# Kernel tuning notes

Hardware: AMD Instinct MI355X
Metric: run time of the kernel (lower is better)

The kernel has to match this reference:

```python
import jax, jax.numpy as jnp
import numpy as np

B, S, E, NH = 2, 2048, 1024, 4
HD = E // NH  # 256


def setup_inputs() -> dict:
    key = jax.random.key(0)
    ks = jax.random.split(key, 8)
    return {
        "q": jax.random.normal(ks[0], (B, S, E), jnp.float32),
        "k": jax.random.normal(ks[1], (B, S, E), jnp.float32),
        "v": jax.random.normal(ks[2], (B, S, E), jnp.float32),
        # gate Dense params (kernel zero-init in the module; use small random for a nontrivial baseline)
        "igate_kernel": jax.random.normal(ks[3], (3 * E, NH), jnp.float32) * 0.02,
        "igate_bias": jax.random.normal(ks[4], (NH,), jnp.float32) * 0.1,
        "fgate_kernel": jax.random.normal(ks[5], (3 * E, NH), jnp.float32) * 0.02,
        "fgate_bias": jnp.linspace(3.0, 6.0, NH, dtype=jnp.float32),  # bias_linspace_init
        "rms_scale": jax.random.normal(ks[6], (HD,), jnp.float32) * 0.02,
    }


def _mlstm_head(q, k, v, ig, fg, eps=1e-06):
    # q,k,v: (S, DH); ig, fg: (S, 1)
    s, dh = q.shape
    log_f = jax.nn.log_sigmoid(fg)                       # (S,1)
    cs = jnp.concatenate([jnp.zeros((1, 1), log_f.dtype),
                          jnp.cumsum(log_f, axis=0)], axis=0)  # (S+1,1)
    neg = jnp.asarray(-0.7 * jnp.finfo(cs.dtype).max, cs.dtype)
    log_d = jnp.where(jnp.tri(s, dtype=bool),
                      (cs - cs.T)[1:, 1:] + ig.T, neg)   # (S,S)
    m = jnp.max(log_d, axis=-1, keepdims=True)           # row-wise stabilizer
    d = jnp.exp(log_d - m)
    c = (q @ (k.T / jnp.sqrt(dh))) * d                   # (S,S)
    n = jnp.maximum(jnp.sum(c, axis=-1, keepdims=True), jnp.exp(-m))
    return (c / (n + eps)) @ v                           # (S,DH)


def reference(q, k, v, igate_kernel, igate_bias, fgate_kernel, fgate_bias, rms_scale):
    b, s, e = q.shape
    nh = igate_kernel.shape[1]
    hd = e // nh
    gate_in = jnp.concatenate((q, k, v), axis=-1)                 # (B,S,3E)
    ig = (gate_in @ igate_kernel + igate_bias).swapaxes(-1, -2)[..., None]  # (B,NH,S,1)
    fg = (gate_in @ fgate_kernel + fgate_bias).swapaxes(-1, -2)[..., None]  # (B,NH,S,1)
    qh = q.reshape(b, s, nh, hd).swapaxes(1, 2)                   # (B,NH,S,HD)
    kh = k.reshape(b, s, nh, hd).swapaxes(1, 2)
    vh = v.reshape(b, s, nh, hd).swapaxes(1, 2)
    h = jax.vmap(jax.vmap(_mlstm_head))(qh, kh, vh, ig, fg)      # (B,NH,S,HD)
    # RMSNorm over head_dim with (1+scale)
    var = jnp.mean(jnp.square(h.astype(jnp.float32)), axis=-1, keepdims=True)
    h = (h * jax.lax.rsqrt(var + 1e-06)).astype(h.dtype) * (1.0 + rms_scale)
    return h.swapaxes(1, 2).reshape(b, s, e)
```

## Files before the change

### kernel.cpp

```cpp
#include <hip/hip_runtime.h>
#include <math.h>

static constexpr int B_  = 2;
static constexpr int S_  = 2048;
static constexpr int E_  = 1024;
static constexpr int NH_ = 4;
static constexpr int HD_ = 256;
static constexpr int BH_ = B_ * NH_;

typedef __attribute__((ext_vector_type(8))) _Float16 half8;
typedef __attribute__((ext_vector_type(4))) float    f32x4;
typedef __attribute__((ext_vector_type(4))) _Float16 half4v;

__global__ __launch_bounds__(1024) void prep_kernel(
    const float* __restrict__ q, const float* __restrict__ k, const float* __restrict__ v,
    const float* __restrict__ igk, const float* __restrict__ igb,
    const float* __restrict__ fgk, const float* __restrict__ fgb,
    float* __restrict__ ig_out, float* __restrict__ fg_out,
    _Float16* __restrict__ Qh, _Float16* __restrict__ Kh, _Float16* __restrict__ Vt)
{
    __shared__ __align__(16) char PSM[98304];
    float4* wi = (float4*)PSM;
    float4* wf = wi + 3 * E_;

    const int t = threadIdx.x;
    #pragma unroll
    for (int i = 0; i < 3; ++i) {
        int e = t + 1024 * i;
        wi[e] = ((const float4*)igk)[e];
        wf[e] = ((const float4*)fgk)[e];
    }
    __syncthreads();

    const int wave = t >> 6;
    const int l    = t & 63;
    const int bs   = blockIdx.x * 16 + wave;
    const int b = bs >> 11, s = bs & (S_ - 1);
    const float* qrow = q + (size_t)bs * E_;
    const float* krow = k + (size_t)bs * E_;
    const float* vrow = v + (size_t)bs * E_;

    float accI[4] = {0.f,0.f,0.f,0.f}, accF[4] = {0.f,0.f,0.f,0.f};
    #pragma unroll
    for (int j = 0; j < 48; ++j) {
        const int e = l + 64 * j;
        float g;
        if (j < 16)       g = qrow[e];
        else if (j < 32)  g = krow[e - E_];
        else              g = vrow[e - 2 * E_];
        if (j < 16) {
            int hh = e >> 8, d = e & 255;
            Qh[(((size_t)(b * NH_ + hh)) * S_ + s) * HD_ + d] = (_Float16)(g * 0.0625f);
        } else if (j < 32) {
            int e2 = e - E_; int hh = e2 >> 8, d = e2 & 255;
            Kh[(((size_t)(b * NH_ + hh)) * S_ + s) * HD_ + d] = (_Float16)g;
        }
        float4 wiv = wi[e];
        float4 wfv = wf[e];
        accI[0] = fmaf(g, wiv.x, accI[0]); accI[1] = fmaf(g, wiv.y, accI[1]);
        accI[2] = fmaf(g, wiv.z, accI[2]); accI[3] = fmaf(g, wiv.w, accI[3]);
        accF[0] = fmaf(g, wfv.x, accF[0]); accF[1] = fmaf(g, wfv.y, accF[1]);
        accF[2] = fmaf(g, wfv.z, accF[2]); accF[3] = fmaf(g, wfv.w, accF[3]);
    }
    #pragma unroll
    for (int m = 1; m < 64; m <<= 1) {
        #pragma unroll
        for (int h = 0; h < 4; ++h) {
            accI[h] += __shfl_xor(accI[h], m);
            accF[h] += __shfl_xor(accF[h], m);
        }
    }
    if (l == 0) {
        #pragma unroll
        for (int h = 0; h < 4; ++h) {
            ig_out[((size_t)(b * NH_ + h)) * S_ + s] = accI[h] + igb[h];
            fg_out[((size_t)(b * NH_ + h)) * S_ + s] = accF[h] + fgb[h];
        }
    }

    __syncthreads();
    {
        float (*tile)[65] = (float(*)[65])(PSM + (t >> 8) * 16640);
        const int tid = t & 255;
        const int m  = blockIdx.x * 4 + (t >> 8);
        const int bh = m & 7;
        const int sb = (m >> 3) & 31;
        const int db = m >> 8;
        const int bb = bh >> 2, hh = bh & 3;
        const int j4 = (tid & 15) * 4;
        const int i0 = tid >> 4;
        const float* src = v + ((size_t)(bb * S_ + sb * 64)) * E_ + hh * HD_ + db * 64;
        #pragma unroll
        for (int p = 0; p < 4; ++p) {
            int i = i0 + p * 16;
            float4 val = *(const float4*)(src + (size_t)i * E_ + j4);
            tile[i][j4] = val.x; tile[i][j4+1] = val.y; tile[i][j4+2] = val.z; tile[i][j4+3] = val.w;
        }
        __syncthreads();
        const int s4 = (tid & 15) * 4;
        const int d0 = tid >> 4;
        _Float16* dst = Vt + ((size_t)bh * HD_ + db * 64) * S_ + sb * 64;
        #pragma unroll
        for (int p = 0; p < 4; ++p) {
            int d = d0 + p * 16;
            half4v pk;
            pk.x = (_Float16)tile[s4][d];   pk.y = (_Float16)tile[s4+1][d];
            pk.z = (_Float16)tile[s4+2][d]; pk.w = (_Float16)tile[s4+3][d];
            *(half4v*)(dst + (size_t)d * S_ + s4) = pk;
        }
    }
}

static constexpr int KSS = 264;
static constexpr int VSS = 72;
static constexpr int PBS = 72;
static constexpr int OFF_VS  = 64 * KSS * 2;
static constexpr int OFF_PB  = OFF_VS + 256 * VSS * 2;
static constexpr int OFF_RSE = OFF_PB + 2 * 16 * PBS * 2;
static constexpr int OFF_SSE = OFF_RSE + 512;
static constexpr int OFF_AMM = OFF_SSE + 512;
static constexpr int OFF_G   = OFF_AMM + S_ * 4;
static constexpr int OFF_M   = OFF_G   + S_ * 4;
static constexpr int SMB     = OFF_M   + S_ * 4;

__global__ __launch_bounds__(512, 2) void mlstm_kernel(
    const _Float16* __restrict__ Qh, const _Float16* __restrict__ Kh,
    const _Float16* __restrict__ Vt,
    const float* __restrict__ ig, const float* __restrict__ fg,
    const float* __restrict__ rms_scale, float* __restrict__ out)
{
    __shared__ __align__(16) char SMEM[SMB];
    _Float16* Ks    = (_Float16*)SMEM;
    _Float16* Vs    = (_Float16*)(SMEM + OFF_VS);
    _Float16* Pb    = (_Float16*)(SMEM + OFF_PB);
    float*    rsumE = (float*)(SMEM + OFF_RSE);
    float*    ssE   = (float*)(SMEM + OFF_SSE);
    float*    sAmM  = (float*)(SMEM + OFF_AMM);
    float*    sG    = (float*)(SMEM + OFF_G);
    float*    sM    = (float*)(SMEM + OFF_M);

    const int z  = blockIdx.x;
    const int bh = z & 7;
    const int u  = z >> 3;
    const int b  = bh >> 2, h = bh & 3;
    const int t  = threadIdx.x;
    const int w  = t >> 6;
    const int l  = t & 63;
    const int col  = l & 15;
    const int quad = l >> 4;
    const int qo   = quad * 8;
    const int rw   = w >> 2;
    const int cq   = w & 3;

    {
        float* sc = (float*)SMEM;
        const float* fgp = fg + (size_t)bh * S_;
        const float* igp = ig + (size_t)bh * S_;
        float ls[4];
        float run = 0.f;
        #pragma unroll
        for (int i = 0; i < 4; ++i) {
            float x = fgp[t * 4 + i];
            float lg = (x >= 0.f) ? -log1pf(expf(-x)) : (x - log1pf(expf(x)));
            run += lg;
            ls[i] = run;
        }
        sc[t] = run;
        __syncthreads();
        for (int off = 1; off < 512; off <<= 1) {
            float vv = (t >= off) ? sc[t - off] : 0.f;
            __syncthreads();
            sc[t] += vv;
            __syncthreads();
        }
        float excl = sc[t] - run;
        float A[4], g[4], gm[4];
        #pragma unroll
        for (int i = 0; i < 4; ++i) A[i] = excl + ls[i];
        float rmax = -__builtin_inff();
        #pragma unroll
        for (int i = 0; i < 4; ++i) {
            g[i] = igp[t * 4 + i] - A[i];
            rmax = fmaxf(rmax, g[i]);
            gm[i] = rmax;
        }
        __syncthreads();
        sc[t] = rmax;
        __syncthreads();
        for (int off = 1; off < 512; off <<= 1) {
            float vv = (t >= off) ? sc[t - off] : -__builtin_inff();
            __syncthreads();
            sc[t] = fmaxf(sc[t], vv);
            __syncthreads();
        }
        float exm = (t == 0) ? -__builtin_inff() : sc[t - 1];
        #pragma unroll
        for (int i = 0; i < 4; ++i) {
            float cm = fmaxf(exm, gm[i]);
            float Mi = A[i] + cm;
            sAmM[t * 4 + i] = A[i] - Mi;
            sG[t * 4 + i]   = g[i];
            sM[t * 4 + i]   = Mi;
        }
        __syncthreads();
    }

    const _Float16* Qp  = Qh + (size_t)bh * S_ * HD_;
    const _Float16* Kp  = Kh + (size_t)bh * S_ * HD_;
    const _Float16* Vtp = Vt + (size_t)bh * HD_ * S_;
    _Float16* Pbr = Pb + rw * 16 * PBS;

    half8 kpre[4], vpre[4];
    auto issueK = [&](int c0n) {
        #pragma unroll
        for (int i = 0; i < 4; ++i) {
            int p = t + 512 * i;
            int row = p >> 5, ck = p & 31;
            kpre[i] = *(const half8*)(Kp + (size_t)(c0n + row) * HD_ + ck * 8);
        }
    };
    auto issueV = [&](int c0n) {
        #pragma unroll
        for (int i = 0; i < 4; ++i) {
            int p = t + 512 * i;
            int n = p >> 3, ch = p & 7;
            vpre[i] = *(const half8*)(Vtp + (size_t)n * S_ + c0n + ch * 8);
        }
    };

    issueK(0);
    issueV(0);

    for (int pass = 0; pass < 2; ++pass) {
        const int rb = pass ? (63 - u) : u;
        const int rowbase = rb * 32 + rw * 16;

        half8 qf[8];
        #pragma unroll
        for (int kk = 0; kk < 8; ++kk)
            qf[kk] = *(const half8*)(Qp + (size_t)(rowbase + col) * HD_ + kk * 32 + qo);
        float amM[4];
        #pragma unroll
        for (int rr = 0; rr < 4; ++rr) amM[rr] = sAmM[rowbase + quad * 4 + rr];

        f32x4 acc[4];
        #pragma unroll
        for (int nn = 0; nn < 4; ++nn) acc[nn] = (f32x4){0.f, 0.f, 0.f, 0.f};
        float rs[4] = {0.f, 0.f, 0.f, 0.f};

        const int Tt = (rb >> 1) + 1;
        for (int jt = 0; jt < Tt; ++jt) {
            const int c0 = jt << 6;
            __syncthreads();
            #pragma unroll
            for (int i = 0; i < 4; ++i) {
                int p = t + 512 * i;
                int row = p >> 5, ck = p & 31;
                *(half8*)(Ks + row * KSS + ck * 8) = kpre[i];
            }
            #pragma unroll
            for (int i = 0; i < 4; ++i) {
                int p = t + 512 * i;
                int n = p >> 3, ch = p & 7;
                *(half8*)(Vs + n * VSS + ch * 8) = vpre[i];
            }
            __syncthreads();
            if (!(pass == 1 && jt + 1 == Tt)) {
                const int cn = (jt + 1 < Tt) ? (c0 + 64) : 0;
                issueK(cn);
                issueV(cn);
            }
            const float gv = sG[c0 + cq * 16 + col];
            f32x4 sc0 = (f32x4){0.f,0.f,0.f,0.f};
            #pragma unroll
            for (int kk = 0; kk < 8; ++kk) {
                half8 kf = *(const half8*)(Ks + (cq * 16 + col) * KSS + kk * 32 + qo);
                sc0 = __builtin_amdgcn_mfma_f32_16x16x32_f16(qf[kk], kf, sc0, 0, 0, 0);
            }
            #pragma unroll
            for (int rr = 0; rr < 4; ++rr) {
                const int ig_ = rowbase + quad * 4 + rr;
                float e0 = __expf(amM[rr] + gv);
                float p0 = (c0 + cq * 16 + col <= ig_) ? sc0[rr] * e0 : 0.f;
                rs[rr] += p0;
                Pbr[(quad * 4 + rr) * PBS + cq * 16 + col] = (_Float16)p0;
            }
            __syncthreads();
            half8 af0 = *(const half8*)(Pbr + col * PBS + qo);
            half8 af1 = *(const half8*)(Pbr + col * PBS + 32 + qo);
            #pragma unroll
            for (int nn = 0; nn < 4; ++nn) {
                const int n = cq * 64 + nn * 16 + col;
                half8 vf0 = *(const half8*)(Vs + n * VSS + qo);
                half8 vf1 = *(const half8*)(Vs + n * VSS + 32 + qo);
                acc[nn] = __builtin_amdgcn_mfma_f32_16x16x32_f16(af0, vf0, acc[nn], 0, 0, 0);
                acc[nn] = __builtin_amdgcn_mfma_f32_16x16x32_f16(af1, vf1, acc[nn], 0, 0, 0);
            }
        }

        #pragma unroll
        for (int m = 1; m < 16; m <<= 1) {
            #pragma unroll
            for (int rr = 0; rr < 4; ++rr) rs[rr] += __shfl_xor(rs[rr], m);
        }
        if (col == 0) {
            #pragma unroll
            for (int rr = 0; rr < 4; ++rr)
                rsumE[rw * 64 + cq * 16 + quad * 4 + rr] = rs[rr];
        }
        __syncthreads();
        float inv[4], ss[4];
        #pragma unroll
        for (int rr = 0; rr < 4; ++rr) {
            const int r = quad * 4 + rr;
            float tot = rsumE[rw * 64 + r] + rsumE[rw * 64 + 16 + r]
                      + rsumE[rw * 64 + 32 + r] + rsumE[rw * 64 + 48 + r];
            float Mv = sM[rowbase + r];
            float n = fmaxf(tot, __expf(-Mv)) + 1e-6f;
            inv[rr] = 1.0f / n;
            ss[rr] = 0.f;
        }
        #pragma unroll
        for (int nn = 0; nn < 4; ++nn) {
            #pragma unroll
            for (int rr = 0; rr < 4; ++rr) {
                float hv = acc[nn][rr] * inv[rr];
                acc[nn][rr] = hv;
                ss[rr] = fmaf(hv, hv, ss[rr]);
            }
        }
        #pragma unroll
        for (int m = 1; m < 16; m <<= 1) {
            #pragma unroll
            for (int rr = 0; rr < 4; ++rr) ss[rr] += __shfl_xor(ss[rr], m);
        }
        if (col == 0) {
            #pragma unroll
            for (int rr = 0; rr < 4; ++rr)
                ssE[rw * 64 + cq * 16 + quad * 4 + rr] = ss[rr];
        }
        __syncthreads();
        #pragma unroll
        for (int rr = 0; rr < 4; ++rr) {
            const int r = quad * 4 + rr;
            float sst = ssE[rw * 64 + r] + ssE[rw * 64 + 16 + r]
                      + ssE[rw * 64 + 32 + r] + ssE[rw * 64 + 48 + r];
            float rstd = rsqrtf(sst * (1.0f / HD_) + 1e-6f);
            float* orow = out + ((size_t)(b * S_ + rowbase + r)) * E_ + h * HD_;
            #pragma unroll
            for (int nn = 0; nn < 4; ++nn) {
                const int c = cq * 64 + nn * 16 + col;
                orow[c] = acc[nn][rr] * rstd * (1.0f + rms_scale[c]);
            }
        }
        __syncthreads();
    }
}

extern "C" void kernel_launch(void* const* d_in, const int* in_sizes, int n_in,
                              void* d_out, int out_size, void* d_ws, size_t ws_size,
                              hipStream_t stream) {
    (void)in_sizes; (void)n_in; (void)out_size; (void)ws_size;
    const float* q   = (const float*)d_in[0];
    const float* k   = (const float*)d_in[1];
    const float* v   = (const float*)d_in[2];
    const float* igk = (const float*)d_in[3];
    const float* igb = (const float*)d_in[4];
    const float* fgk = (const float*)d_in[5];
    const float* fgb = (const float*)d_in[6];
    const float* rsc = (const float*)d_in[7];
    float* out = (float*)d_out;

    float* ws  = (float*)d_ws;
    float* ig  = ws;
    float* fg  = ws + (size_t)BH_ * S_;
    _Float16* Qh = (_Float16*)(ws + (size_t)2 * BH_ * S_);
    _Float16* Kh = Qh + (size_t)BH_ * S_ * HD_;
    _Float16* Vt = Kh + (size_t)BH_ * S_ * HD_;

    prep_kernel<<<B_ * S_ / 16, 1024, 0, stream>>>(q, k, v, igk, igb, fgk, fgb,
                                                   ig, fg, Qh, Kh, Vt);
    mlstm_kernel<<<BH_ * 32, 512, 0, stream>>>(Qh, Kh, Vt, ig, fg, rsc, out);
}
```

Before: 168.5 us.

## Split prep kernel into gate-projection blocks and V-transpose blocks with register-blocked rows

The prep kernel is restructured from 256 blocks of 1024 threads, each staging 96KB of gate weights in shared memory, into 2048 blocks of 256 threads. The first 1024 blocks each compute gate projections for 4 rows using float4 vector loads, read the weights straight from global/cache with reuse across the 4 rows in registers, and reduce across waves through a small shared buffer. The remaining 1024 blocks do the V transpose on their own. This is meant to cut the shared-memory weight staging and raise occupancy and load vectorisation, at the cost of re-reading the weights from cache in every block.

```diff
diff --git a/kernel.cpp b/kernel.cpp
--- a/kernel.cpp
+++ b/kernel.cpp
@@ -12,77 +12,110 @@
 typedef __attribute__((ext_vector_type(4))) float    f32x4;
 typedef __attribute__((ext_vector_type(4))) _Float16 half4v;
 
-__global__ __launch_bounds__(1024) void prep_kernel(
+__global__ __launch_bounds__(256) void prep_kernel(
     const float* __restrict__ q, const float* __restrict__ k, const float* __restrict__ v,
     const float* __restrict__ igk, const float* __restrict__ igb,
     const float* __restrict__ fgk, const float* __restrict__ fgb,
     float* __restrict__ ig_out, float* __restrict__ fg_out,
     _Float16* __restrict__ Qh, _Float16* __restrict__ Kh, _Float16* __restrict__ Vt)
 {
-    __shared__ __align__(16) char PSM[98304];
-    float4* wi = (float4*)PSM;
-    float4* wf = wi + 3 * E_;
-
-    const int t = threadIdx.x;
-    #pragma unroll
-    for (int i = 0; i < 3; ++i) {
-        int e = t + 1024 * i;
-        wi[e] = ((const float4*)igk)[e];
-        wf[e] = ((const float4*)fgk)[e];
-    }
-    __syncthreads();
-
-    const int wave = t >> 6;
-    const int l    = t & 63;
-    const int bs   = blockIdx.x * 16 + wave;
-    const int b = bs >> 11, s = bs & (S_ - 1);
-    const float* qrow = q + (size_t)bs * E_;
-    const float* krow = k + (size_t)bs * E_;
-    const float* vrow = v + (size_t)bs * E_;
-
-    float accI[4] = {0.f,0.f,0.f,0.f}, accF[4] = {0.f,0.f,0.f,0.f};
-    #pragma unroll
-    for (int j = 0; j < 48; ++j) {
-        const int e = l + 64 * j;
-        float g;
-        if (j < 16)       g = qrow[e];
-        else if (j < 32)  g = krow[e - E_];
-        else              g = vrow[e - 2 * E_];
-        if (j < 16) {
-            int hh = e >> 8, d = e & 255;
-            Qh[(((size_t)(b * NH_ + hh)) * S_ + s) * HD_ + d] = (_Float16)(g * 0.0625f);
-        } else if (j < 32) {
-            int e2 = e - E_; int hh = e2 >> 8, d = e2 & 255;
-            Kh[(((size_t)(b * NH_ + hh)) * S_ + s) * HD_ + d] = (_Float16)g;
-        }
-        float4 wiv = wi[e];
-        float4 wfv = wf[e];
-        accI[0] = fmaf(g, wiv.x, accI[0]); accI[1] = fmaf(g, wiv.y, accI[1]);
-        accI[2] = fmaf(g, wiv.z, accI[2]); accI[3] = fmaf(g, wiv.w, accI[3]);
-        accF[0] = fmaf(g, wfv.x, accF[0]); accF[1] = fmaf(g, wfv.y, accF[1]);
-        accF[2] = fmaf(g, wfv.z, accF[2]); accF[3] = fmaf(g, wfv.w, accF[3]);
-    }
-    #pragma unroll
-    for (int m = 1; m < 64; m <<= 1) {
-        #pragma unroll
-        for (int h = 0; h < 4; ++h) {
-            accI[h] += __shfl_xor(accI[h], m);
-            accF[h] += __shfl_xor(accF[h], m);
-        }
-    }
-    if (l == 0) {
-        #pragma unroll
-        for (int h = 0; h < 4; ++h) {
-            ig_out[((size_t)(b * NH_ + h)) * S_ + s] = accI[h] + igb[h];
-            fg_out[((size_t)(b * NH_ + h)) * S_ + s] = accF[h] + fgb[h];
-        }
-    }
-
-    __syncthreads();
-    {
-        float (*tile)[65] = (float(*)[65])(PSM + (t >> 8) * 16640);
-        const int tid = t & 255;
-        const int m  = blockIdx.x * 4 + (t >> 8);
+    __shared__ __align__(16) char PSM[16640];
+    const int tid = threadIdx.x;
+
+    if (blockIdx.x < 1024) {
+        const int bs0 = blockIdx.x * 4;
+        const float4* w_i = (const float4*)igk;
+        const float4* w_f = (const float4*)fgk;
+
+        float accI[4][4], accF[4][4];
+        #pragma unroll
+        for (int r = 0; r < 4; ++r)
+            #pragma unroll
+            for (int h = 0; h < 4; ++h) { accI[r][h] = 0.f; accF[r][h] = 0.f; }
+
+        #pragma unroll
+        for (int it = 0; it < 3; ++it) {
+            const int e4  = tid + 256 * it;
+            const int e4l = e4 & 255;
+            const float* src = (it == 0) ? q : (it == 1) ? k : v;
+
+            float4 g4[4];
+            #pragma unroll
+            for (int r = 0; r < 4; ++r)
+                g4[r] = ((const float4*)(src + (size_t)(bs0 + r) * E_))[e4l];
+
+            if (it == 0) {
+                #pragma unroll
+                for (int r = 0; r < 4; ++r) {
+                    const int bs = bs0 + r, b = bs >> 11, s = bs & (S_ - 1);
+                    half4v hq = { (_Float16)(g4[r].x * 0.0625f), (_Float16)(g4[r].y * 0.0625f),
+                                  (_Float16)(g4[r].z * 0.0625f), (_Float16)(g4[r].w * 0.0625f) };
+                    *(half4v*)(Qh + ((size_t)(b * NH_ + (e4l >> 6)) * S_ + s) * HD_ + (e4l & 63) * 4) = hq;
+                }
+            } else if (it == 1) {
+                #pragma unroll
+                for (int r = 0; r < 4; ++r) {
+                    const int bs = bs0 + r, b = bs >> 11, s = bs & (S_ - 1);
+                    half4v hk = { (_Float16)g4[r].x, (_Float16)g4[r].y,
+                                  (_Float16)g4[r].z, (_Float16)g4[r].w };
+                    *(half4v*)(Kh + ((size_t)(b * NH_ + (e4l >> 6)) * S_ + s) * HD_ + (e4l & 63) * 4) = hk;
+                }
+            }
+
+            float4 wi4[4], wf4[4];
+            #pragma unroll
+            for (int j = 0; j < 4; ++j) {
+                wi4[j] = w_i[e4 * 4 + j];
+                wf4[j] = w_f[e4 * 4 + j];
+            }
+            #pragma unroll
+            for (int r = 0; r < 4; ++r) {
+                const float gx[4] = { g4[r].x, g4[r].y, g4[r].z, g4[r].w };
+                #pragma unroll
+                for (int j = 0; j < 4; ++j) {
+                    accI[r][0] = fmaf(gx[j], wi4[j].x, accI[r][0]);
+                    accI[r][1] = fmaf(gx[j], wi4[j].y, accI[r][1]);
+                    accI[r][2] = fmaf(gx[j], wi4[j].z, accI[r][2]);
+                    accI[r][3] = fmaf(gx[j], wi4[j].w, accI[r][3]);
+                    accF[r][0] = fmaf(gx[j], wf4[j].x, accF[r][0]);
+                    accF[r][1] = fmaf(gx[j], wf4[j].y, accF[r][1]);
+                    accF[r][2] = fmaf(gx[j], wf4[j].z, accF[r][2]);
+                    accF[r][3] = fmaf(gx[j], wf4[j].w, accF[r][3]);
+                }
+            }
+        }
+        #pragma unroll
+        for (int m = 1; m < 64; m <<= 1) {
+            #pragma unroll
+            for (int r = 0; r < 4; ++r)
+                #pragma unroll
+                for (int h = 0; h < 4; ++h) {
+                    accI[r][h] += __shfl_xor(accI[r][h], m);
+                    accF[r][h] += __shfl_xor(accF[r][h], m);
+                }
+        }
+        float (*red)[4][8] = (float(*)[4][8])PSM;
+        const int wave = tid >> 6;
+        if ((tid & 63) == 0) {
+            #pragma unroll
+            for (int r = 0; r < 4; ++r)
+                #pragma unroll
+                for (int h = 0; h < 4; ++h) {
+                    red[wave][r][h]     = accI[r][h];
+                    red[wave][r][4 + h] = accF[r][h];
+                }
+        }
+        __syncthreads();
+        if (tid < 32) {
+            const int r = tid >> 3, c = tid & 7, h = c & 3;
+            float sum = red[0][r][c] + red[1][r][c] + red[2][r][c] + red[3][r][c];
+            const int bs = bs0 + r, b = bs >> 11, s = bs & (S_ - 1);
+            if (c < 4) ig_out[((size_t)(b * NH_ + h)) * S_ + s] = sum + igb[h];
+            else       fg_out[((size_t)(b * NH_ + h)) * S_ + s] = sum + fgb[h];
+        }
+    } else {
+        float (*tile)[65] = (float(*)[65])PSM;
+        const int m  = blockIdx.x - 1024;
         const int bh = m & 7;
         const int sb = (m >> 3) & 31;
         const int db = m >> 8;
@@ -378,7 +411,7 @@
     _Float16* Kh = Qh + (size_t)BH_ * S_ * HD_;
     _Float16* Vt = Kh + (size_t)BH_ * S_ * HD_;
 
-    prep_kernel<<<B_ * S_ / 16, 1024, 0, stream>>>(q, k, v, igk, igb, fgk, fgb,
-                                                   ig, fg, Qh, Kh, Vt);
+    prep_kernel<<<2048, 256, 0, stream>>>(q, k, v, igk, igb, fgk, fgb,
+                                          ig, fg, Qh, Kh, Vt);
     mlstm_kernel<<<BH_ * 32, 512, 0, stream>>>(Qh, Kh, Vt, ig, fg, rsc, out);
 }
```

After: 175.5 us. +4.1%, slower.
